# Kernel tuning notes

Hardware: AMD Instinct MI355X
Metric: run time of the kernel (lower is better)

The kernel has to match this reference:

```python
import jax, jax.numpy as jnp
import numpy as np

# --- constants matching the torch module's default-camera / material / light setup ---
IMAGE_SIZE = 128
SCALE = 1.0
FOCAL = 12.0
R_MAT = jnp.array([[-1.0, 0.0, 0.0], [0.0, 1.0, 0.0], [0.0, 0.0, -1.0]], dtype=jnp.float32)
T_VEC = jnp.array([0.0, 0.0, 2.0 * SCALE], dtype=jnp.float32)
CAM_POS = jnp.array([0.0, 0.0, 2.0 * SCALE], dtype=jnp.float32)  # camera center in world coords
LIGHT_LOC = jnp.array([0.0, 1.0, 3.0], dtype=jnp.float32)
AMB_L, DIFF_L, SPEC_L = 0.5, 0.3, 0.2          # PointLights defaults
MAT_AMB, MAT_DIFF, MAT_SPEC = 1.0, 1.0, 0.6    # Materials(specular_color=0.6)
SHININESS = 10.0
TEXEL = jnp.array([142.0, 179.0, 247.0], dtype=jnp.float32) / 255.0  # uniform vertex color
BG = 1.0  # BlendParams background
EPS = 1e-8


def _normalize(v):
    return v / (jnp.linalg.norm(v, axis=-1, keepdims=True) + EPS)


def _render_one(verts, faces):
    """verts: [V,3] world space; faces: [F,3] int. Returns ([3,H,W] rgb*255, [1,H,W] alpha)."""
    H = W = IMAGE_SIZE
    # world -> view (PyTorch3D row-vector convention: x_view = x @ R + T)
    view = verts @ R_MAT + T_VEC              # [V,3]
    z = view[:, 2]                            # [V] view-space depth (>0 in front)
    ndc = FOCAL * view[:, :2] / z[:, None]    # [V,2] perspective projection to NDC
    tri = ndc[faces]                          # [F,3,2]
    tz = z[faces]                             # [F,3]

    # pixel centers in NDC (PyTorch3D: +x left, +y up)
    xs = 1.0 - (2.0 * jnp.arange(W) + 1.0) / W
    ys = 1.0 - (2.0 * jnp.arange(H) + 1.0) / H
    gy, gx = jnp.meshgrid(ys, xs, indexing='ij')
    px = gx.reshape(-1).astype(jnp.float32)   # [P]
    py = gy.reshape(-1).astype(jnp.float32)   # [P]

    v0, v1, v2 = tri[:, 0], tri[:, 1], tri[:, 2]   # [F,2]

    def edge(a, b):  # signed area cross(b-a, p-a) for all pixels -> [P,F]
        return ((b[:, 0] - a[:, 0])[None] * (py[:, None] - a[:, 1][None])
                - (b[:, 1] - a[:, 1])[None] * (px[:, None] - a[:, 0][None]))

    area = ((v1[:, 0] - v0[:, 0]) * (v2[:, 1] - v0[:, 1])
            - (v1[:, 1] - v0[:, 1]) * (v2[:, 0] - v0[:, 0]))   # [F]
    area_safe = jnp.where(jnp.abs(area) < EPS, EPS, area)
    b0 = edge(v1, v2) / area_safe             # [P,F]
    b1 = edge(v2, v0) / area_safe
    b2 = 1.0 - b0 - b1
    inside = (b0 >= 0) & (b1 >= 0) & (b2 >= 0) & (jnp.abs(area) > EPS)[None]

    # perspective-correct interpolated depth: z_pix = 1 / sum_i(b_i / z_i)
    S = b0 / tz[:, 0] + b1 / tz[:, 1] + b2 / tz[:, 2]
    depth = jnp.where(inside & (S > EPS), 1.0 / jnp.maximum(S, EPS), jnp.inf)
    fidx = jnp.argmin(depth, axis=1)          # [P] z-buffer winner (faces_per_pixel=1)
    hit = jnp.isfinite(jnp.min(depth, axis=1))

    # --- recompute barycentrics only for the winning face per pixel (cheap, [P]) ---
    f = faces[fidx]                           # [P,3]
    tv = ndc[f]                               # [P,3,2]
    tzp = z[f]                                # [P,3]
    a0, a1, a2 = tv[:, 0], tv[:, 1], tv[:, 2]

    def edge_p(a, b):
        return (b[:, 0] - a[:, 0]) * (py - a[:, 1]) - (b[:, 1] - a[:, 1]) * (px - a[:, 0])

    ar = (a1[:, 0] - a0[:, 0]) * (a2[:, 1] - a0[:, 1]) - (a1[:, 1] - a0[:, 1]) * (a2[:, 0] - a0[:, 0])
    ar = jnp.where(jnp.abs(ar) < EPS, EPS, ar)
    bb0 = edge_p(a1, a2) / ar
    bb1 = edge_p(a2, a0) / ar
    bb2 = 1.0 - bb0 - bb1
    w = jnp.stack([bb0 / tzp[:, 0], bb1 / tzp[:, 1], bb2 / tzp[:, 2]], axis=-1)
    pc = w / (jnp.sum(w, axis=-1, keepdims=True) + EPS)   # [P,3] perspective-correct barycentrics

    # --- vertex normals (world space) ---
    fv = verts[faces]                         # [F,3,3]
    fn = jnp.cross(fv[:, 1] - fv[:, 0], fv[:, 2] - fv[:, 0])  # [F,3]
    vn = (jnp.zeros_like(verts)
          .at[faces[:, 0]].add(fn)
          .at[faces[:, 1]].add(fn)
          .at[faces[:, 2]].add(fn))
    vn = _normalize(vn)

    # --- interpolate position/normal, Phong shade ---
    pos = jnp.einsum('pk,pkd->pd', pc, verts[f])   # [P,3]
    nrm = _normalize(jnp.einsum('pk,pkd->pd', pc, vn[f]))
    l = _normalize(LIGHT_LOC - pos)
    vdir = _normalize(CAM_POS - pos)
    ndl = jax.nn.relu(jnp.sum(nrm * l, axis=-1))          # [P]
    refl = 2.0 * jnp.sum(nrm * l, axis=-1, keepdims=True) * nrm - l
    spec_cos = jax.nn.relu(jnp.sum(refl * vdir, axis=-1))
    ambient = AMB_L * MAT_AMB
    diffuse = DIFF_L * MAT_DIFF * ndl
    specular = SPEC_L * MAT_SPEC * spec_cos ** SHININESS
    color = TEXEL[None] * (ambient + diffuse[:, None]) + specular[:, None]

    rgb = jnp.where(hit[:, None], color, BG)              # hard blend with white bg
    alpha = hit.astype(verts.dtype)
    img = rgb.reshape(H, W, 3).transpose(2, 0, 1) * 255.0  # [3,H,W]
    a = alpha.reshape(1, H, W)
    return img, a


def setup_inputs() -> dict:
    key = jax.random.key(0)
    k1, k2 = jax.random.split(key)
    B, V, F = 2, 1300, 2500
    vertices = jax.random.normal(k1, (B, V, 3), dtype=jnp.float32) * 0.05  # head-scale mesh near origin
    faces = jax.random.randint(k2, (F, 3), 0, V, dtype=jnp.int32)
    return {"vertices": vertices, "faces": faces}


def reference(vertices, faces):
    # ori_size == image_size, so the area-interpolation in the torch module is the identity.
    images, alphas = jax.lax.map(lambda v: _render_one(v, faces), vertices)
    return images, alphas
```

## Files before the change

kernel.cpp:

```cpp
#include <hip/hip_runtime.h>
#include <math.h>

#pragma clang fp contract(off)

#define IMG_H 128
#define IMG_W 128
#define HW (IMG_H * IMG_W)
#define NB 2
#define NV 1300
#define NF 2500
#define EPSF 1e-8f
#define NCHUNK 32
#define CHUNK ((NF + NCHUNK - 1) / NCHUNK)
#define NREG 128
#define NBLK (NREG * NB * NCHUNK)

#define OFF_FACE 31232
#define OFF_DBUF 351488

#define DINIT 0x7F800000FFFFFFFFull

__global__ __launch_bounds__(256) void k_face(const float* __restrict__ verts,
                                              const int* __restrict__ faces,
                                              float* __restrict__ vn,
                                              float4* __restrict__ face) {
    int i = blockIdx.x * 256 + threadIdx.x;
    if (i >= NB * NF) return;
    int b = i / NF;
    int f = i - b * NF;
    int i0 = faces[f * 3 + 0];
    int i1 = faces[f * 3 + 1];
    int i2 = faces[f * 3 + 2];
    const float* wv = verts + (size_t)b * NV * 3;
    float v0x = wv[i0 * 3 + 0], v0y = wv[i0 * 3 + 1], v0z = wv[i0 * 3 + 2];
    float v1x = wv[i1 * 3 + 0], v1y = wv[i1 * 3 + 1], v1z = wv[i1 * 3 + 2];
    float v2x = wv[i2 * 3 + 0], v2y = wv[i2 * 3 + 1], v2z = wv[i2 * 3 + 2];
    float z0 = 2.0f - v0z, z1 = 2.0f - v1z, z2 = 2.0f - v2z;
    float p0x = (12.0f * (-v0x)) / z0, p0y = (12.0f * v0y) / z0;
    float p1x = (12.0f * (-v1x)) / z1, p1y = (12.0f * v1y) / z1;
    float p2x = (12.0f * (-v2x)) / z2, p2y = (12.0f * v2y) / z2;

    float t1 = (p1x - p0x) * (p2y - p0y);
    float t2 = (p1y - p0y) * (p2x - p0x);
    float area = t1 - t2;
    float aabs = fabsf(area);
    float area_safe = (aabs < EPSF) ? EPSF : area;
    bool valid = aabs > EPSF;
    float minx, maxx, miny, maxy;
    if (valid) {
        minx = fminf(p0x, fminf(p1x, p2x)) - 1e-3f;
        maxx = fmaxf(p0x, fmaxf(p1x, p2x)) + 1e-3f;
        miny = fminf(p0y, fminf(p1y, p2y)) - 1e-3f;
        maxy = fmaxf(p0y, fmaxf(p1y, p2y)) + 1e-3f;
    } else {
        minx = 1e30f; maxx = -1e30f; miny = 1e30f; maxy = -1e30f;
    }
    int o = (b * NF + f) * 4;
    face[o + 0] = make_float4(p2x - p1x, p2y - p1y, p1x, p1y);
    face[o + 1] = make_float4(p0x - p2x, p0y - p2y, p2x, p2y);
    face[o + 2] = make_float4(area_safe, z0, z1, z2);
    face[o + 3] = make_float4(minx, maxx, miny, maxy);

    float ax = v1x - v0x, ay = v1y - v0y, az = v1z - v0z;
    float bx = v2x - v0x, by = v2y - v0y, bz = v2z - v0z;
    float fnx = ay * bz - az * by;
    float fny = az * bx - ax * bz;
    float fnz = ax * by - ay * bx;
    float* vnb = vn + (size_t)b * NV * 3;
    atomicAdd(&vnb[i0 * 3 + 0], fnx);
    atomicAdd(&vnb[i0 * 3 + 1], fny);
    atomicAdd(&vnb[i0 * 3 + 2], fnz);
    atomicAdd(&vnb[i1 * 3 + 0], fnx);
    atomicAdd(&vnb[i1 * 3 + 1], fny);
    atomicAdd(&vnb[i1 * 3 + 2], fnz);
    atomicAdd(&vnb[i2 * 3 + 0], fnx);
    atomicAdd(&vnb[i2 * 3 + 1], fny);
    atomicAdd(&vnb[i2 * 3 + 2], fnz);
}

__global__ __launch_bounds__(128) void k_raster(const float4* __restrict__ face,
                                                unsigned long long* __restrict__ dbuf) {
    __shared__ float4 sface[CHUNK * 4];
    __shared__ int sidx[CHUNK];
    __shared__ int swbase[2];
    __shared__ int scnt;

    int bx = blockIdx.x;
    int chunk = bx & (NCHUNK - 1);
    int tmp = bx >> 5;
    int b = tmp & 1;
    int reg = tmp >> 1;
    int r0 = (reg >> 3) * 8;
    int c0 = (reg & 7) * 16;
    int f0 = chunk * CHUNK;
    int nf = NF - f0; if (nf > CHUNK) nf = CHUNK;

    float txmax = 1.0f - (2.0f * (float)c0 + 1.0f) / 128.0f;
    float txmin = 1.0f - (2.0f * (float)(c0 + 15) + 1.0f) / 128.0f;
    float tymax = 1.0f - (2.0f * (float)r0 + 1.0f) / 128.0f;
    float tymin = 1.0f - (2.0f * (float)(r0 + 7) + 1.0f) / 128.0f;

    const float4* fb = face + (size_t)b * NF * 4;
    int t = threadIdx.x;
    int wid = t >> 6, lid = t & 63;
    bool pass = false;
    float4 bb;
    if (t < nf) {
        bb = fb[(f0 + t) * 4 + 3];
        pass = (bb.y >= txmin) && (bb.x <= txmax) && (bb.w >= tymin) && (bb.z <= tymax);
    }
    unsigned long long m = __ballot(pass);
    if (lid == 0) swbase[wid] = __popcll(m);
    __syncthreads();
    int base0 = swbase[0];
    if (pass) {
        int pos = (wid ? base0 : 0) + __popcll(m & ((1ull << lid) - 1ull));
        sface[pos * 4 + 0] = fb[(f0 + t) * 4 + 0];
        sface[pos * 4 + 1] = fb[(f0 + t) * 4 + 1];
        sface[pos * 4 + 2] = fb[(f0 + t) * 4 + 2];
        sface[pos * 4 + 3] = bb;
        sidx[pos] = f0 + t;
    }
    if (t == 0) scnt = base0 + swbase[1];
    __syncthreads();
    int cnt = scnt;

    int r = r0 + (lid >> 3);
    int c = c0 + wid * 8 + (lid & 7);
    int p = r * IMG_W + c;
    float px = 1.0f - (2.0f * (float)c + 1.0f) / 128.0f;
    float py = 1.0f - (2.0f * (float)r + 1.0f) / 128.0f;

    unsigned long long best = DINIT;
    for (int j = 0; j < cnt; ++j) {
        float4 fbb = sface[j * 4 + 3];
        if (px >= fbb.x && px <= fbb.y && py >= fbb.z && py <= fbb.w) {
            float4 E0 = sface[j * 4 + 0];
            float4 E1 = sface[j * 4 + 1];
            float4 FD = sface[j * 4 + 2];
            float u1 = E0.x * (py - E0.w);
            float u2 = E0.y * (px - E0.z);
            float e0 = u1 - u2;
            float u3 = E1.x * (py - E1.w);
            float u4 = E1.y * (px - E1.z);
            float e1 = u3 - u4;
            float as = FD.x;
            bool ok = (as > 0.0f) ? (e0 >= 0.0f && e1 >= 0.0f)
                                  : (e0 <= 0.0f && e1 <= 0.0f);
            if (ok) {
                float b0 = e0 / as;
                float b1 = e1 / as;
                float b2 = (1.0f - b0) - b1;
                if (b2 >= 0.0f) {
                    float S = ((b0 / FD.y) + (b1 / FD.z)) + (b2 / FD.w);
                    if (S > EPSF) {
                        float depth = 1.0f / fmaxf(S, EPSF);
                        unsigned long long pk =
                            ((unsigned long long)__float_as_uint(depth) << 32) |
                            (unsigned)sidx[j];
                        if (pk < best) best = pk;
                    }
                }
            }
        }
    }
    dbuf[((size_t)chunk * NB + b) * HW + p] = best;
}

__global__ __launch_bounds__(256) void k_shade(const float* __restrict__ verts,
                                               const int* __restrict__ faces,
                                               const float* __restrict__ vn,
                                               const unsigned long long* __restrict__ dbuf,
                                               float* __restrict__ out) {
    int i = blockIdx.x * 256 + threadIdx.x;
    int b = i >> 14;
    int p = i & (HW - 1);
    unsigned long long pk = DINIT;
    for (int k = 0; k < NCHUNK; ++k) {
        unsigned long long v = dbuf[((size_t)k * NB + b) * HW + p];
        if (v < pk) pk = v;
    }
    unsigned dbits = (unsigned)(pk >> 32);
    bool hit = dbits < 0x7F800000u;
    float cr = 255.0f, cg = 255.0f, cb = 255.0f, alpha = 0.0f;
    if (hit) {
        alpha = 1.0f;
        int f = (int)(unsigned)(pk & 0xFFFFFFFFull);
        int row = p >> 7;
        int col = p & 127;
        float px = 1.0f - (2.0f * (float)col + 1.0f) / 128.0f;
        float py = 1.0f - (2.0f * (float)row + 1.0f) / 128.0f;
        int i0 = faces[f * 3 + 0];
        int i1 = faces[f * 3 + 1];
        int i2 = faces[f * 3 + 2];
        const float* wv = verts + (size_t)b * NV * 3;
        float v0x = wv[i0 * 3 + 0], v0y = wv[i0 * 3 + 1], v0z = wv[i0 * 3 + 2];
        float v1x = wv[i1 * 3 + 0], v1y = wv[i1 * 3 + 1], v1z = wv[i1 * 3 + 2];
        float v2x = wv[i2 * 3 + 0], v2y = wv[i2 * 3 + 1], v2z = wv[i2 * 3 + 2];
        float z0 = 2.0f - v0z, z1 = 2.0f - v1z, z2 = 2.0f - v2z;
        float a0x = (12.0f * (-v0x)) / z0, a0y = (12.0f * v0y) / z0;
        float a1x = (12.0f * (-v1x)) / z1, a1y = (12.0f * v1y) / z1;
        float a2x = (12.0f * (-v2x)) / z2, a2y = (12.0f * v2y) / z2;

        float t1 = (a1x - a0x) * (a2y - a0y);
        float t2 = (a1y - a0y) * (a2x - a0x);
        float ar = t1 - t2;
        ar = (fabsf(ar) < EPSF) ? EPSF : ar;
        float u1 = (a2x - a1x) * (py - a1y);
        float u2 = (a2y - a1y) * (px - a1x);
        float bb0 = (u1 - u2) / ar;
        float u3 = (a0x - a2x) * (py - a2y);
        float u4 = (a0y - a2y) * (px - a2x);
        float bb1 = (u3 - u4) / ar;
        float bb2 = (1.0f - bb0) - bb1;
        float w0 = bb0 / z0;
        float w1 = bb1 / z1;
        float w2 = bb2 / z2;
        float denom = ((w0 + w1) + w2) + EPSF;
        float pc0 = w0 / denom;
        float pc1 = w1 / denom;
        float pc2 = w2 / denom;

        float posx = (pc0 * v0x + pc1 * v1x) + pc2 * v2x;
        float posy = (pc0 * v0y + pc1 * v1y) + pc2 * v2y;
        float posz = (pc0 * v0z + pc1 * v1z) + pc2 * v2z;

        const float* vnb = vn + (size_t)b * NV * 3;
        float n0x = vnb[i0 * 3 + 0], n0y = vnb[i0 * 3 + 1], n0z = vnb[i0 * 3 + 2];
        float n1x = vnb[i1 * 3 + 0], n1y = vnb[i1 * 3 + 1], n1z = vnb[i1 * 3 + 2];
        float n2x = vnb[i2 * 3 + 0], n2y = vnb[i2 * 3 + 1], n2z = vnb[i2 * 3 + 2];
        float in0 = 1.0f / (sqrtf(n0x * n0x + n0y * n0y + n0z * n0z) + EPSF);
        float in1 = 1.0f / (sqrtf(n1x * n1x + n1y * n1y + n1z * n1z) + EPSF);
        float in2 = 1.0f / (sqrtf(n2x * n2x + n2y * n2y + n2z * n2z) + EPSF);
        n0x *= in0; n0y *= in0; n0z *= in0;
        n1x *= in1; n1y *= in1; n1z *= in1;
        n2x *= in2; n2y *= in2; n2z *= in2;
        float nx = (pc0 * n0x + pc1 * n1x) + pc2 * n2x;
        float ny = (pc0 * n0y + pc1 * n1y) + pc2 * n2y;
        float nz = (pc0 * n0z + pc1 * n1z) + pc2 * n2z;
        float inn = 1.0f / (sqrtf(nx * nx + ny * ny + nz * nz) + EPSF);
        nx *= inn; ny *= inn; nz *= inn;

        float lx = 0.0f - posx, ly = 1.0f - posy, lz = 3.0f - posz;
        float iln = 1.0f / (sqrtf(lx * lx + ly * ly + lz * lz) + EPSF);
        lx *= iln; ly *= iln; lz *= iln;
        float vx = 0.0f - posx, vy = 0.0f - posy, vz = 2.0f - posz;
        float ivn = 1.0f / (sqrtf(vx * vx + vy * vy + vz * vz) + EPSF);
        vx *= ivn; vy *= ivn; vz *= ivn;

        float ndl = nx * lx + ny * ly + nz * lz;
        float ndlr = fmaxf(ndl, 0.0f);
        float rx = 2.0f * ndl * nx - lx;
        float ry = 2.0f * ndl * ny - ly;
        float rz = 2.0f * ndl * nz - lz;
        float sc = fmaxf(rx * vx + ry * vy + rz * vz, 0.0f);
        float spec = 0.2f * 0.6f * powf(sc, 10.0f);
        float shade = 0.5f * 1.0f + 0.3f * 1.0f * ndlr;
        cr = ((142.0f / 255.0f) * shade + spec) * 255.0f;
        cg = ((179.0f / 255.0f) * shade + spec) * 255.0f;
        cb = ((247.0f / 255.0f) * shade + spec) * 255.0f;
    }
    float* img = out + (size_t)b * 3 * HW;
    img[0 * HW + p] = cr;
    img[1 * HW + p] = cg;
    img[2 * HW + p] = cb;
    out[(size_t)NB * 3 * HW + (size_t)b * HW + p] = alpha;
}

extern "C" void kernel_launch(void* const* d_in, const int* in_sizes, int n_in,
                              void* d_out, int out_size, void* d_ws, size_t ws_size,
                              hipStream_t stream) {
    const float* verts = (const float*)d_in[0];
    const int* faces = (const int*)d_in[1];
    char* ws = (char*)d_ws;
    float* vn = (float*)(ws + 0);
    float4* face = (float4*)(ws + OFF_FACE);
    unsigned long long* dbuf = (unsigned long long*)(ws + OFF_DBUF);
    float* out = (float*)d_out;

    hipMemsetAsync(vn, 0, NB * NV * 3 * sizeof(float), stream);
    k_face<<<(NB * NF + 255) / 256, 256, 0, stream>>>(verts, faces, vn, face);
    k_raster<<<NBLK, 128, 0, stream>>>(face, dbuf);
    k_shade<<<(NB * HW) / 256, 256, 0, stream>>>(verts, faces, vn, dbuf, out);
}
```

Measured before the change: 103.5 us.

## Replace tile-by-face-chunk rasterization with per-face binned tasks and atomicMin z-buffer

```diff
diff --git a/kernel.cpp b/kernel.cpp
--- a/kernel.cpp
+++ b/kernel.cpp
@@ -3,168 +3,155 @@
 
 #pragma clang fp contract(off)
 
-#define IMG_H 128
-#define IMG_W 128
-#define HW (IMG_H * IMG_W)
+#define IMG 128
+#define HW (IMG * IMG)
 #define NB 2
 #define NV 1300
 #define NF 2500
+#define NFACE (NB * NF)
 #define EPSF 1e-8f
-#define NCHUNK 32
-#define CHUNK ((NF + NCHUNK - 1) / NCHUNK)
-#define NREG 128
-#define NBLK (NREG * NB * NCHUNK)
-
-#define OFF_FACE 31232
-#define OFF_DBUF 351488
-
-#define DINIT 0x7F800000FFFFFFFFull
+#define MAXTASK 80000
+#define NWAVE 4096
+
+#define OFF_CNT 31232
+#define OFF_FACE 31744
+#define OFF_RECT 271744
+#define OFF_TASK 351744
+#define OFF_DBUF 671744
 
 __global__ __launch_bounds__(256) void k_face(const float* __restrict__ verts,
                                               const int* __restrict__ faces,
                                               float* __restrict__ vn,
-                                              float4* __restrict__ face) {
+                                              float4* __restrict__ face,
+                                              int4* __restrict__ rect,
+                                              unsigned* __restrict__ task,
+                                              int* __restrict__ cnt) {
     int i = blockIdx.x * 256 + threadIdx.x;
-    if (i >= NB * NF) return;
-    int b = i / NF;
-    int f = i - b * NF;
-    int i0 = faces[f * 3 + 0];
-    int i1 = faces[f * 3 + 1];
-    int i2 = faces[f * 3 + 2];
-    const float* wv = verts + (size_t)b * NV * 3;
-    float v0x = wv[i0 * 3 + 0], v0y = wv[i0 * 3 + 1], v0z = wv[i0 * 3 + 2];
-    float v1x = wv[i1 * 3 + 0], v1y = wv[i1 * 3 + 1], v1z = wv[i1 * 3 + 2];
-    float v2x = wv[i2 * 3 + 0], v2y = wv[i2 * 3 + 1], v2z = wv[i2 * 3 + 2];
-    float z0 = 2.0f - v0z, z1 = 2.0f - v1z, z2 = 2.0f - v2z;
-    float p0x = (12.0f * (-v0x)) / z0, p0y = (12.0f * v0y) / z0;
-    float p1x = (12.0f * (-v1x)) / z1, p1y = (12.0f * v1y) / z1;
-    float p2x = (12.0f * (-v2x)) / z2, p2y = (12.0f * v2y) / z2;
-
-    float t1 = (p1x - p0x) * (p2y - p0y);
-    float t2 = (p1y - p0y) * (p2x - p0x);
-    float area = t1 - t2;
-    float aabs = fabsf(area);
-    float area_safe = (aabs < EPSF) ? EPSF : area;
-    bool valid = aabs > EPSF;
-    float minx, maxx, miny, maxy;
-    if (valid) {
-        minx = fminf(p0x, fminf(p1x, p2x)) - 1e-3f;
-        maxx = fmaxf(p0x, fmaxf(p1x, p2x)) + 1e-3f;
-        miny = fminf(p0y, fminf(p1y, p2y)) - 1e-3f;
-        maxy = fmaxf(p0y, fmaxf(p1y, p2y)) + 1e-3f;
-    } else {
-        minx = 1e30f; maxx = -1e30f; miny = 1e30f; maxy = -1e30f;
-    }
-    int o = (b * NF + f) * 4;
-    face[o + 0] = make_float4(p2x - p1x, p2y - p1y, p1x, p1y);
-    face[o + 1] = make_float4(p0x - p2x, p0y - p2y, p2x, p2y);
-    face[o + 2] = make_float4(area_safe, z0, z1, z2);
-    face[o + 3] = make_float4(minx, maxx, miny, maxy);
-
-    float ax = v1x - v0x, ay = v1y - v0y, az = v1z - v0z;
-    float bx = v2x - v0x, by = v2y - v0y, bz = v2z - v0z;
-    float fnx = ay * bz - az * by;
-    float fny = az * bx - ax * bz;
-    float fnz = ax * by - ay * bx;
-    float* vnb = vn + (size_t)b * NV * 3;
-    atomicAdd(&vnb[i0 * 3 + 0], fnx);
-    atomicAdd(&vnb[i0 * 3 + 1], fny);
-    atomicAdd(&vnb[i0 * 3 + 2], fnz);
-    atomicAdd(&vnb[i1 * 3 + 0], fnx);
-    atomicAdd(&vnb[i1 * 3 + 1], fny);
-    atomicAdd(&vnb[i1 * 3 + 2], fnz);
-    atomicAdd(&vnb[i2 * 3 + 0], fnx);
-    atomicAdd(&vnb[i2 * 3 + 1], fny);
-    atomicAdd(&vnb[i2 * 3 + 2], fnz);
-}
-
-__global__ __launch_bounds__(128) void k_raster(const float4* __restrict__ face,
+    int lane = threadIdx.x & 63;
+    bool act = i < NFACE;
+    int nb = 0;
+    int cmin = 0, cmax = 0, rmin = 0, rmax = 0;
+    if (act) {
+        int b = (i >= NF) ? 1 : 0;
+        int f = i - b * NF;
+        int i0 = faces[f * 3 + 0];
+        int i1 = faces[f * 3 + 1];
+        int i2 = faces[f * 3 + 2];
+        const float* wv = verts + (size_t)b * NV * 3;
+        float v0x = wv[i0 * 3 + 0], v0y = wv[i0 * 3 + 1], v0z = wv[i0 * 3 + 2];
+        float v1x = wv[i1 * 3 + 0], v1y = wv[i1 * 3 + 1], v1z = wv[i1 * 3 + 2];
+        float v2x = wv[i2 * 3 + 0], v2y = wv[i2 * 3 + 1], v2z = wv[i2 * 3 + 2];
+        float z0 = 2.0f - v0z, z1 = 2.0f - v1z, z2 = 2.0f - v2z;
+        float p0x = (12.0f * (-v0x)) / z0, p0y = (12.0f * v0y) / z0;
+        float p1x = (12.0f * (-v1x)) / z1, p1y = (12.0f * v1y) / z1;
+        float p2x = (12.0f * (-v2x)) / z2, p2y = (12.0f * v2y) / z2;
+
+        float t1 = (p1x - p0x) * (p2y - p0y);
+        float t2 = (p1y - p0y) * (p2x - p0x);
+        float area = t1 - t2;
+        float aabs = fabsf(area);
+        float area_safe = (aabs < EPSF) ? EPSF : area;
+
+        face[i * 3 + 0] = make_float4(p2x - p1x, p2y - p1y, p1x, p1y);
+        face[i * 3 + 1] = make_float4(p0x - p2x, p0y - p2y, p2x, p2y);
+        face[i * 3 + 2] = make_float4(area_safe, z0, z1, z2);
+
+        if (aabs > EPSF) {
+            float minx = fminf(p0x, fminf(p1x, p2x));
+            float maxx = fmaxf(p0x, fmaxf(p1x, p2x));
+            float miny = fminf(p0y, fminf(p1y, p2y));
+            float maxy = fmaxf(p0y, fmaxf(p1y, p2y));
+            int ci0 = (int)floorf((1.0f - maxx) * 64.0f - 0.5f) - 1;
+            int ci1 = (int)floorf((1.0f - minx) * 64.0f - 0.5f) + 1;
+            int ri0 = (int)floorf((1.0f - maxy) * 64.0f - 0.5f) - 1;
+            int ri1 = (int)floorf((1.0f - miny) * 64.0f - 0.5f) + 1;
+            if (ci1 >= 0 && ci0 <= 127 && ri1 >= 0 && ri0 <= 127) {
+                cmin = max(ci0, 0); cmax = min(ci1, 127);
+                rmin = max(ri0, 0); rmax = min(ri1, 127);
+                nb = ((rmax - rmin) >> 3) + 1;
+            }
+        }
+        rect[i] = make_int4(cmin, cmax, rmin, rmax);
+
+        float ax = v1x - v0x, ay = v1y - v0y, az = v1z - v0z;
+        float bx = v2x - v0x, by = v2y - v0y, bz = v2z - v0z;
+        float fnx = ay * bz - az * by;
+        float fny = az * bx - ax * bz;
+        float fnz = ax * by - ay * bx;
+        float* vnb = vn + (size_t)b * NV * 3;
+        atomicAdd(&vnb[i0 * 3 + 0], fnx);
+        atomicAdd(&vnb[i0 * 3 + 1], fny);
+        atomicAdd(&vnb[i0 * 3 + 2], fnz);
+        atomicAdd(&vnb[i1 * 3 + 0], fnx);
+        atomicAdd(&vnb[i1 * 3 + 1], fny);
+        atomicAdd(&vnb[i1 * 3 + 2], fnz);
+        atomicAdd(&vnb[i2 * 3 + 0], fnx);
+        atomicAdd(&vnb[i2 * 3 + 1], fny);
+        atomicAdd(&vnb[i2 * 3 + 2], fnz);
+    }
+    int incl = nb;
+    for (int d = 1; d < 64; d <<= 1) {
+        int v = __shfl_up(incl, d, 64);
+        if (lane >= d) incl += v;
+    }
+    int wtot = __shfl(incl, 63, 64);
+    int wbase = 0;
+    if (lane == 0 && wtot > 0) wbase = atomicAdd(cnt, wtot);
+    wbase = __shfl(wbase, 0, 64);
+    int my0 = wbase + incl - nb;
+    for (int k = 0; k < nb; ++k) task[my0 + k] = (unsigned)i | ((unsigned)k << 16);
+}
+
+__global__ __launch_bounds__(256) void k_raster(const float4* __restrict__ face,
+                                                const int4* __restrict__ rect,
+                                                const unsigned* __restrict__ task,
+                                                const int* __restrict__ cnt,
                                                 unsigned long long* __restrict__ dbuf) {
-    __shared__ float4 sface[CHUNK * 4];
-    __shared__ int sidx[CHUNK];
-    __shared__ int swbase[2];
-    __shared__ int scnt;
-
-    int bx = blockIdx.x;
-    int chunk = bx & (NCHUNK - 1);
-    int tmp = bx >> 5;
-    int b = tmp & 1;
-    int reg = tmp >> 1;
-    int r0 = (reg >> 3) * 8;
-    int c0 = (reg & 7) * 16;
-    int f0 = chunk * CHUNK;
-    int nf = NF - f0; if (nf > CHUNK) nf = CHUNK;
-
-    float txmax = 1.0f - (2.0f * (float)c0 + 1.0f) / 128.0f;
-    float txmin = 1.0f - (2.0f * (float)(c0 + 15) + 1.0f) / 128.0f;
-    float tymax = 1.0f - (2.0f * (float)r0 + 1.0f) / 128.0f;
-    float tymin = 1.0f - (2.0f * (float)(r0 + 7) + 1.0f) / 128.0f;
-
-    const float4* fb = face + (size_t)b * NF * 4;
-    int t = threadIdx.x;
-    int wid = t >> 6, lid = t & 63;
-    bool pass = false;
-    float4 bb;
-    if (t < nf) {
-        bb = fb[(f0 + t) * 4 + 3];
-        pass = (bb.y >= txmin) && (bb.x <= txmax) && (bb.w >= tymin) && (bb.z <= tymax);
-    }
-    unsigned long long m = __ballot(pass);
-    if (lid == 0) swbase[wid] = __popcll(m);
-    __syncthreads();
-    int base0 = swbase[0];
-    if (pass) {
-        int pos = (wid ? base0 : 0) + __popcll(m & ((1ull << lid) - 1ull));
-        sface[pos * 4 + 0] = fb[(f0 + t) * 4 + 0];
-        sface[pos * 4 + 1] = fb[(f0 + t) * 4 + 1];
-        sface[pos * 4 + 2] = fb[(f0 + t) * 4 + 2];
-        sface[pos * 4 + 3] = bb;
-        sidx[pos] = f0 + t;
-    }
-    if (t == 0) scnt = base0 + swbase[1];
-    __syncthreads();
-    int cnt = scnt;
-
-    int r = r0 + (lid >> 3);
-    int c = c0 + wid * 8 + (lid & 7);
-    int p = r * IMG_W + c;
-    float px = 1.0f - (2.0f * (float)c + 1.0f) / 128.0f;
-    float py = 1.0f - (2.0f * (float)r + 1.0f) / 128.0f;
-
-    unsigned long long best = DINIT;
-    for (int j = 0; j < cnt; ++j) {
-        float4 fbb = sface[j * 4 + 3];
-        if (px >= fbb.x && px <= fbb.y && py >= fbb.z && py <= fbb.w) {
-            float4 E0 = sface[j * 4 + 0];
-            float4 E1 = sface[j * 4 + 1];
-            float4 FD = sface[j * 4 + 2];
+    int lane = threadIdx.x & 63;
+    int wave = blockIdx.x * 4 + (threadIdx.x >> 6);
+    int n = *cnt;
+    int lr = lane >> 3, lc = lane & 7;
+    for (int t = wave; t < n; t += NWAVE) {
+        unsigned tk = task[t];
+        int i = (int)(tk & 0xFFFFu);
+        int band = (int)(tk >> 16);
+        int4 rc = rect[i];
+        float4 E0 = face[i * 3 + 0];
+        float4 E1 = face[i * 3 + 1];
+        float4 FD = face[i * 3 + 2];
+        int b = (i >= NF) ? 1 : 0;
+        int f = i - b * NF;
+        float as = FD.x;
+        int r = rc.z + (band << 3) + lr;
+        bool vr = (r <= rc.w);
+        float py = 1.0f - (2.0f * (float)r + 1.0f) / 128.0f;
+        unsigned long long* db = dbuf + (size_t)b * HW;
+        for (int cb = rc.x; cb <= rc.y; cb += 8) {
+            int c = cb + lc;
+            bool v = vr && (c <= rc.y);
+            float px = 1.0f - (2.0f * (float)c + 1.0f) / 128.0f;
             float u1 = E0.x * (py - E0.w);
             float u2 = E0.y * (px - E0.z);
             float e0 = u1 - u2;
             float u3 = E1.x * (py - E1.w);
             float u4 = E1.y * (px - E1.z);
             float e1 = u3 - u4;
-            float as = FD.x;
-            bool ok = (as > 0.0f) ? (e0 >= 0.0f && e1 >= 0.0f)
-                                  : (e0 <= 0.0f && e1 <= 0.0f);
-            if (ok) {
+            bool ok = v && ((as > 0.0f) ? (e0 >= 0.0f && e1 >= 0.0f)
+                                        : (e0 <= 0.0f && e1 <= 0.0f));
+            if (__any(ok)) {
                 float b0 = e0 / as;
                 float b1 = e1 / as;
                 float b2 = (1.0f - b0) - b1;
-                if (b2 >= 0.0f) {
-                    float S = ((b0 / FD.y) + (b1 / FD.z)) + (b2 / FD.w);
-                    if (S > EPSF) {
-                        float depth = 1.0f / fmaxf(S, EPSF);
-                        unsigned long long pk =
-                            ((unsigned long long)__float_as_uint(depth) << 32) |
-                            (unsigned)sidx[j];
-                        if (pk < best) best = pk;
-                    }
+                float S = ((b0 / FD.y) + (b1 / FD.z)) + (b2 / FD.w);
+                if (ok && b2 >= 0.0f && S > EPSF) {
+                    float depth = 1.0f / fmaxf(S, EPSF);
+                    unsigned long long pk =
+                        ((unsigned long long)__float_as_uint(depth) << 32) | (unsigned)f;
+                    atomicMin(&db[r * IMG + c], pk);
                 }
             }
         }
     }
-    dbuf[((size_t)chunk * NB + b) * HW + p] = best;
 }
 
 __global__ __launch_bounds__(256) void k_shade(const float* __restrict__ verts,
@@ -175,11 +162,7 @@
     int i = blockIdx.x * 256 + threadIdx.x;
     int b = i >> 14;
     int p = i & (HW - 1);
-    unsigned long long pk = DINIT;
-    for (int k = 0; k < NCHUNK; ++k) {
-        unsigned long long v = dbuf[((size_t)k * NB + b) * HW + p];
-        if (v < pk) pk = v;
-    }
+    unsigned long long pk = dbuf[i];
     unsigned dbits = (unsigned)(pk >> 32);
     bool hit = dbits < 0x7F800000u;
     float cr = 255.0f, cg = 255.0f, cb = 255.0f, alpha = 0.0f;
@@ -274,12 +257,16 @@
     const int* faces = (const int*)d_in[1];
     char* ws = (char*)d_ws;
     float* vn = (float*)(ws + 0);
+    int* cnt = (int*)(ws + OFF_CNT);
     float4* face = (float4*)(ws + OFF_FACE);
+    int4* rect = (int4*)(ws + OFF_RECT);
+    unsigned* task = (unsigned*)(ws + OFF_TASK);
     unsigned long long* dbuf = (unsigned long long*)(ws + OFF_DBUF);
     float* out = (float*)d_out;
 
-    hipMemsetAsync(vn, 0, NB * NV * 3 * sizeof(float), stream);
-    k_face<<<(NB * NF + 255) / 256, 256, 0, stream>>>(verts, faces, vn, face);
-    k_raster<<<NBLK, 128, 0, stream>>>(face, dbuf);
+    hipMemsetAsync(ws, 0, OFF_CNT + 4, stream);
+    hipMemsetAsync(ws + OFF_DBUF, 0xFF, NB * HW * 8, stream);
+    k_face<<<(NFACE + 255) / 256, 256, 0, stream>>>(verts, faces, vn, face, rect, task, cnt);
+    k_raster<<<NWAVE / 4, 256, 0, stream>>>(face, rect, task, cnt, dbuf);
     k_shade<<<(NB * HW) / 256, 256, 0, stream>>>(verts, faces, vn, dbuf, out);
 }
```

Result: slower. 110.1 us (+6.4%).
